# Performance work log

Measured on AMD Instinct MI355X. Metric: run time of the kernel, lower is better.

The kernel has to match this reference:

```python
import jax, jax.numpy as jnp
import numpy as np

N_ANGLES = 8


def setup_inputs() -> dict:
    key = jax.random.key(0)
    ks = jax.random.split(key, 6)
    N, in_size, out_size, K = 20000, 64, 64, 8
    M = N_ANGLES * N            # block-Laplacian dim = 160000
    E = M * 16                  # avg degree 16 -> 2.56M nnz
    x = jax.random.normal(ks[0], (N, in_size), dtype=jnp.float32)
    ls_vals = jax.random.normal(ks[1], (E,), dtype=jnp.float32) * 0.1
    ls_rows = jax.random.randint(ks[2], (E,), 0, M, dtype=jnp.int32)
    ls_cols = jax.random.randint(ks[3], (E,), 0, M, dtype=jnp.int32)
    weight = jax.random.normal(ks[4], (K, N_ANGLES * in_size, out_size), dtype=jnp.float32) * 0.05
    bias = jnp.zeros((out_size,), dtype=jnp.float32)
    return {"x": x, "ls_vals": ls_vals, "weight": weight, "bias": bias,
            "ls_rows": ls_rows, "ls_cols": ls_cols}


def reference(x, ls_vals, weight, bias, ls_rows, ls_cols):
    N, in_size = x.shape
    K = weight.shape[0]
    M = N_ANGLES * N

    def spmm(T):
        # sparse [M,M] @ dense [M,in] via gather + segment_sum
        return jax.ops.segment_sum(ls_vals[:, None] * T[ls_cols], ls_rows,
                                   num_segments=M)

    def feat(T):
        # [n_angles*N, in] -> [N, n_angles*in] (angle-major per node)
        return T.reshape(N_ANGLES, N, in_size).transpose(1, 0, 2).reshape(N, -1)

    Tx0 = jnp.tile(x, (N_ANGLES, 1))                  # [M, in]
    out = feat(Tx0) @ weight[0]                       # [N, out]
    Tx1 = spmm(Tx0)
    out = out + feat(Tx1) @ weight[1]
    for k in range(2, K):
        Tx2 = 2.0 * spmm(Tx1) - Tx0
        out = out + feat(Tx2) @ weight[k]
        Tx0, Tx1 = Tx1, Tx2
    return out + bias
```

## Files before the change

kernel.cpp:

```cpp
#include <hip/hip_runtime.h>
#include <hip/hip_bf16.h>

#define N_NODES 20000
#define NANG 8
#define CH 64
#define M_ROWS (NANG * N_NODES)
#define E_EDGES (M_ROWS * 16)
#define K_CHEB 8
#define WK_STRIDE (NANG * CH * CH)
#define BROWS 256
#define NB (M_ROWS / BROWS)
#define NCHUNK 512
#define CHUNK (E_EDGES / NCHUNK)
#define SCAN_K (NCHUNK / 256)
#define SC_RE 20
#define RPW 4
#define SPMM_BLOCKS (M_ROWS / (4 * RPW))
#define KCAT 3648
#define SK_TOTAL 114
#define BCAP 5120
#define GROWS 32
#define GEMM_BLOCKS (N_NODES / GROWS)

typedef short short8 __attribute__((ext_vector_type(8)));
typedef float f32x4 __attribute__((ext_vector_type(4)));

__device__ __forceinline__ float bf2f(ushort u) {
    return __uint_as_float((unsigned int)u << 16);
}


__global__ __launch_bounds__(256) void count_kernel(const int* __restrict__ rows,
                                                    int* __restrict__ chunk_cnt) {
    __shared__ int h[NB];
    int c = blockIdx.x, tid = threadIdx.x;
    for (int i = tid; i < NB; i += 256) h[i] = 0;
    __syncthreads();
    int base = c * CHUNK;
    for (int i = tid; i < CHUNK; i += 256) atomicAdd(&h[rows[base + i] >> 8], 1);
    __syncthreads();
    for (int i = tid; i < NB; i += 256) chunk_cnt[(size_t)c * NB + i] = h[i];
}

__global__ __launch_bounds__(256) void bscan2_kernel(int* __restrict__ chunk_cnt,
                                                     int* __restrict__ btotal) {
    __shared__ int s[256];
    int b = blockIdx.x, t = threadIdx.x;
    int loc[SCAN_K];
    int sum = 0;
#pragma unroll
    for (int k = 0; k < SCAN_K; ++k) {
        loc[k] = chunk_cnt[(size_t)(t * SCAN_K + k) * NB + b];
        sum += loc[k];
    }
    s[t] = sum;
    __syncthreads();
#pragma unroll
    for (int off = 1; off < 256; off <<= 1) {
        int u = (t >= off) ? s[t - off] : 0;
        __syncthreads();
        s[t] += u;
        __syncthreads();
    }
    int run = s[t] - sum;
#pragma unroll
    for (int k = 0; k < SCAN_K; ++k) {
        chunk_cnt[(size_t)(t * SCAN_K + k) * NB + b] = run;
        run += loc[k];
    }
    if (t == 255) btotal[b] = s[255];
}

__global__ void bscan_kernel(const int* __restrict__ btotal, int* __restrict__ bstart) {
    __shared__ int s[1024];
    int t = threadIdx.x;
    int v = (t < NB) ? btotal[t] : 0;
    s[t] = v;
    __syncthreads();
    for (int off = 1; off < 1024; off <<= 1) {
        int u = (t >= off) ? s[t - off] : 0;
        __syncthreads();
        s[t] += u;
        __syncthreads();
    }
    if (t < NB) bstart[t] = s[t] - v;
    if (t == 1023) bstart[NB] = s[1023];
}


__global__ __launch_bounds__(256) void scatter_kernel(
        const int* __restrict__ rows, const int* __restrict__ cols,
        const float* __restrict__ vals, const int* __restrict__ chunk_cnt,
        const int* __restrict__ bstart, int2* __restrict__ bedges) {
    __shared__ int2 stage[CHUNK];
    __shared__ ushort bkey[CHUNK];
    __shared__ int hist[NB];
    __shared__ int fill[NB];
    __shared__ int gaddr[NB];
    __shared__ int sc[256];
    int c = blockIdx.x, tid = threadIdx.x;
    for (int i = tid; i < NB; i += 256) hist[i] = 0;
    __syncthreads();

    int base = c * CHUNK;
    int2 eds[SC_RE];
    int keys[SC_RE];
#pragma unroll
    for (int k = 0; k < SC_RE; ++k) {
        int i = tid + k * 256;
        if (i < CHUNK) {
            int e = base + i;
            int r = rows[e];
            eds[k] = make_int2(cols[e] | ((r & 255) << 18), __float_as_int(vals[e]));
            keys[k] = r >> 8;
            atomicAdd(&hist[keys[k]], 1);
        } else keys[k] = -1;
    }
    __syncthreads();

    int loc[3];
    int sum = 0;
    int b0 = tid * 3;
#pragma unroll
    for (int k = 0; k < 3; ++k) {
        int b = b0 + k;
        loc[k] = (b < NB) ? hist[b] : 0;
        sum += loc[k];
    }
    sc[tid] = sum;
    __syncthreads();
#pragma unroll
    for (int off = 1; off < 256; off <<= 1) {
        int u = (tid >= off) ? sc[tid - off] : 0;
        __syncthreads();
        sc[tid] += u;
        __syncthreads();
    }
    int run = sc[tid] - sum;
#pragma unroll
    for (int k = 0; k < 3; ++k) {
        int b = b0 + k;
        if (b < NB) {
            fill[b] = run;
            gaddr[b] = bstart[b] + chunk_cnt[(size_t)c * NB + b] - run;
        }
        run += loc[k];
    }
    __syncthreads();

#pragma unroll
    for (int k = 0; k < SC_RE; ++k) {
        if (keys[k] >= 0) {
            int p = atomicAdd(&fill[keys[k]], 1);
            stage[p] = eds[k];
            bkey[p] = (ushort)keys[k];
        }
    }
    __syncthreads();

    for (int i = tid; i < CHUNK; i += 256) {
        int b = bkey[i];
        bedges[gaddr[b] + i] = stage[i];
    }
}

__global__ __launch_bounds__(256) void bucket_group_kernel(
        const int* __restrict__ bstart, const int2* __restrict__ bin,
        int2* __restrict__ bout, int* __restrict__ row_start) {
    __shared__ int cnt[BROWS];
    __shared__ int pref[BROWS];
    __shared__ int fill[BROWS];
    __shared__ int2 ob[BCAP];
    int b = blockIdx.x, tid = threadIdx.x;
    int s = bstart[b], e = bstart[b + 1];
    int n = e - s;
    cnt[tid] = 0;
    __syncthreads();
    int2 eds[20];
    int ni = 0;
    for (int i = tid; i < n; i += 256, ++ni) {
        int2 ed = bin[s + i];
        if (ni < 20) eds[ni] = ed;
        atomicAdd(&cnt[(ed.x >> 18) & 255], 1);
    }
    __syncthreads();
    int v = cnt[tid];
    pref[tid] = v;
    __syncthreads();
#pragma unroll
    for (int off = 1; off < 256; off <<= 1) {
        int u = (tid >= off) ? pref[tid - off] : 0;
        __syncthreads();
        pref[tid] += u;
        __syncthreads();
    }
    int my_excl = pref[tid] - v;
    __syncthreads();
    pref[tid] = my_excl;
    fill[tid] = my_excl;
    __syncthreads();

    if (n <= BCAP) {
        ni = 0;
        for (int i = tid; i < n; i += 256, ++ni) {
            int2 ed = (ni < 20) ? eds[ni] : bin[s + i];
            int p = atomicAdd(&fill[(ed.x >> 18) & 255], 1);
            ob[p] = make_int2(ed.x & 0x3ffff, ed.y);
        }
        __syncthreads();
        for (int i = tid; i < n; i += 256)
            bout[s + i] = ob[i];
    } else {
        ni = 0;
        for (int i = tid; i < n; i += 256, ++ni) {
            int2 ed = (ni < 20) ? eds[ni] : bin[s + i];
            int p = atomicAdd(&fill[(ed.x >> 18) & 255], 1);
            bout[s + p] = make_int2(ed.x & 0x3ffff, ed.y);
        }
    }
    row_start[b * BROWS + tid] = s + pref[tid];
    if (b == NB - 1 && tid == 0) row_start[M_ROWS] = e;
}


__global__ void xconv_kernel(const float* __restrict__ x, ushort* __restrict__ xb) {
    int i = blockIdx.x * 256 + threadIdx.x;
    __hip_bfloat16 v = __float2bfloat16(x[i]);
    xb[i] = *(ushort*)&v;
}

__global__ void wcat_kernel(const float* __restrict__ W, ushort* __restrict__ Wcat) {
    int idx = blockIdx.x * 256 + threadIdx.x;
    int n   = idx / KCAT;
    int kkc = idx - n * KCAT;
    float v;
    if (kkc < 64) {
        v = 0.f;
#pragma unroll
        for (int a = 0; a < NANG; ++a) v += W[(a * 64 + kkc) * 64 + n];
    } else {
        int k  = ((kkc - 64) >> 9) + 1;
        int kk = (kkc - 64) & 511;
        v = W[(size_t)k * WK_STRIDE + kk * 64 + n];
    }
    __hip_bfloat16 b = __float2bfloat16(v);
    Wcat[idx] = *(ushort*)&b;
}


template <int TIN_TILED, int TSUB_MODE>
__global__ __launch_bounds__(256) void spmm_kernel(
        const int* __restrict__ row_start, const int2* __restrict__ edges,
        const ushort* __restrict__ Tin, const ushort* __restrict__ Tsub,
        ushort* __restrict__ Tout, float alpha, float beta) {
    int wid = (blockIdx.x * 256 + threadIdx.x) >> 6;
    int lane = threadIdx.x & 63;
    int r0 = wid * RPW;
    int l16 = lane & 15;

    int sb[RPW + 1];
#pragma unroll
    for (int j = 0; j <= RPW; ++j)
        sb[j] = __builtin_amdgcn_readfirstlane(row_start[r0 + j]);

    int2 ed[RPW];
#pragma unroll
    for (int j = 0; j < RPW; ++j) {
        int idx = min(sb[j] + l16, sb[j + 1] - 1);
        idx = max(idx, 0);
        ed[j] = edges[idx];
    }

#pragma unroll
    for (int j = 0; j < RPW; ++j) {
        int s = sb[j], e = sb[j + 1];
        float acc0 = 0.f, acc1 = 0.f;
        int2 cur = ed[j];
        for (int base = s; base < e; base += 16) {
            int2 nxt = cur;
            if (base + 16 < e) {
                int idx = min(base + 16 + l16, e - 1);
                nxt = edges[idx];
            }
            ushort raw[16];
#pragma unroll
            for (int i = 0; i < 16; ++i) {
                unsigned c = (unsigned)__builtin_amdgcn_readlane(cur.x, i);
                if (TIN_TILED) c %= N_NODES;
                raw[i] = Tin[(size_t)c * CH + lane];
            }
#pragma unroll
            for (int i = 0; i < 16; ++i) {
                int wbits = __builtin_amdgcn_readlane(cur.y, i);
                if (base + i >= e) wbits = 0;
                float t = bf2f(raw[i]);
                if (i & 1) acc1 = fmaf(__int_as_float(wbits), t, acc1);
                else       acc0 = fmaf(__int_as_float(wbits), t, acc0);
            }
            cur = nxt;
        }
        int r = r0 + j;
        float v = alpha * (acc0 + acc1);
        size_t oi = (size_t)r * CH + lane;
        if (TSUB_MODE == 1) v += beta * bf2f(Tsub[oi]);
        if (TSUB_MODE == 2) v += beta * bf2f(Tsub[(size_t)((unsigned)r % N_NODES) * CH + lane]);
        __hip_bfloat16 o = __float2bfloat16(v);
        Tout[oi] = *(ushort*)&o;
    }
}


__global__ __launch_bounds__(256) void gemm_cat_kernel(
        const ushort* __restrict__ xb,
        const ushort* __restrict__ Tall,
        const ushort* __restrict__ Wcat,
        const float* __restrict__ bias,
        float* __restrict__ out) {
    __shared__ float red[4][16][64];
    int m0 = blockIdx.x * GROWS;
    int w = threadIdx.x >> 6;
    int l = threadIdx.x & 63;
    int lm = l & 15;
    int lq = l >> 4;
    const short* Xp = (const short*)xb;
    const short* Tp = (const short*)Tall;
    const short* Wp = (const short*)Wcat;

    f32x4 acc[2][4];
#pragma unroll
    for (int rg = 0; rg < 2; ++rg)
#pragma unroll
        for (int t = 0; t < 4; ++t) acc[rg][t] = (f32x4){0.f, 0.f, 0.f, 0.f};

    auto LDA = [&](int sk, int rg) -> short8 {
        int u = sk - 2;
        return *(const short8*)(Tp
            + ((size_t)(u >> 4) * M_ROWS + (size_t)((u & 15) >> 1) * N_NODES
               + (m0 + rg * 16 + lm)) * CH
            + (u & 1) * 32 + lq * 8);
    };
    auto LDB = [&](int sk, int t) -> short8 {
        return *(const short8*)(Wp + (size_t)(t * 16 + lm) * KCAT + sk * 32 + lq * 8);
    };

    if (w == 0) {
#pragma unroll
        for (int sk = 0; sk < 2; ++sk) {
            short8 a0 = *(const short8*)(Xp + (size_t)(m0 + lm) * CH + sk * 32 + lq * 8);
            short8 a1 = *(const short8*)(Xp + (size_t)(m0 + 16 + lm) * CH + sk * 32 + lq * 8);
#pragma unroll
            for (int t = 0; t < 4; ++t) {
                short8 bf = LDB(sk, t);
                acc[0][t] = __builtin_amdgcn_mfma_f32_16x16x32_bf16(a0, bf, acc[0][t], 0, 0, 0);
                acc[1][t] = __builtin_amdgcn_mfma_f32_16x16x32_bf16(a1, bf, acc[1][t], 0, 0, 0);
            }
        }
    }

    int tb = 2 + w * 28;
#pragma unroll 2
    for (int i = 0; i < 28; ++i) {
        int sk = tb + i;
        short8 a0 = LDA(sk, 0);
        short8 a1 = LDA(sk, 1);
#pragma unroll
        for (int t = 0; t < 4; ++t) {
            short8 bf = LDB(sk, t);
            acc[0][t] = __builtin_amdgcn_mfma_f32_16x16x32_bf16(a0, bf, acc[0][t], 0, 0, 0);
            acc[1][t] = __builtin_amdgcn_mfma_f32_16x16x32_bf16(a1, bf, acc[1][t], 0, 0, 0);
        }
    }

#pragma unroll
    for (int rg = 0; rg < 2; ++rg) {
        if (rg) __syncthreads();
#pragma unroll
        for (int t = 0; t < 4; ++t)
#pragma unroll
            for (int rI = 0; rI < 4; ++rI) red[w][t * 4 + rI][l] = acc[rg][t][rI];
        __syncthreads();
        int col = w * 16 + lm;
        float b = bias[col];
#pragma unroll
        for (int rI = 0; rI < 4; ++rI) {
            int i2 = w * 4 + rI;
            float sum = red[0][i2][l] + red[1][i2][l] + red[2][i2][l] + red[3][i2][l];
            out[(size_t)(m0 + rg * 16 + lq * 4 + rI) * CH + col] = sum + b;
        }
    }
}


extern "C" void kernel_launch(void* const* d_in, const int* in_sizes, int n_in,
                              void* d_out, int out_size, void* d_ws, size_t ws_size,
                              hipStream_t stream) {
    (void)in_sizes; (void)n_in; (void)out_size; (void)ws_size;
    const float* x       = (const float*)d_in[0];
    const float* ls_vals = (const float*)d_in[1];
    const float* weight  = (const float*)d_in[2];
    const float* bias    = (const float*)d_in[3];
    const int*   ls_rows = (const int*)d_in[4];
    const int*   ls_cols = (const int*)d_in[5];
    float* out = (float*)d_out;

    char* ws = (char*)d_ws;
    size_t off = 0;
    auto alloc = [&](size_t bytes) -> void* {
        void* p = ws + off;
        off += (bytes + 255) & ~(size_t)255;
        return p;
    };
    int*  chunk_cnt = (int*)alloc((size_t)NCHUNK * NB * sizeof(int));
    int*  btotal    = (int*)alloc(NB * sizeof(int));
    int*  bstart    = (int*)alloc((NB + 1) * sizeof(int));
    int*  row_start = (int*)alloc((M_ROWS + 1) * sizeof(int));
    int2* bedges2   = (int2*)alloc((size_t)E_EDGES * sizeof(int2));
    ushort* Wcat = (ushort*)alloc((size_t)64 * KCAT * sizeof(ushort));
    ushort* xb   = (ushort*)alloc((size_t)N_NODES * CH * sizeof(ushort));
    ushort* Tall = (ushort*)alloc((size_t)7 * M_ROWS * CH * sizeof(ushort));
    int2* bedges = (int2*)Tall;

    count_kernel<<<NCHUNK, 256, 0, stream>>>(ls_rows, chunk_cnt);
    bscan2_kernel<<<NB, 256, 0, stream>>>(chunk_cnt, btotal);
    bscan_kernel<<<1, 1024, 0, stream>>>(btotal, bstart);
    scatter_kernel<<<NCHUNK, 256, 0, stream>>>(ls_rows, ls_cols, ls_vals, chunk_cnt,
                                               bstart, bedges);
    bucket_group_kernel<<<NB, 256, 0, stream>>>(bstart, bedges, bedges2, row_start);

    xconv_kernel<<<(N_NODES * CH) / 256, 256, 0, stream>>>(x, xb);
    wcat_kernel<<<(64 * KCAT) / 256, 256, 0, stream>>>(weight, Wcat);

    ushort* T[8];
    for (int k = 1; k < K_CHEB; ++k) T[k] = Tall + (size_t)(k - 1) * M_ROWS * CH;

    spmm_kernel<1, 0><<<SPMM_BLOCKS, 256, 0, stream>>>(
        row_start, bedges2, xb, xb, T[1], 1.f, 0.f);
    spmm_kernel<0, 2><<<SPMM_BLOCKS, 256, 0, stream>>>(
        row_start, bedges2, T[1], xb, T[2], 2.f, -1.f);
    for (int k = 3; k < K_CHEB; ++k) {
        spmm_kernel<0, 1><<<SPMM_BLOCKS, 256, 0, stream>>>(
            row_start, bedges2, T[k - 1], T[k - 2], T[k], 2.f, -1.f);
    }

    gemm_cat_kernel<<<GEMM_BLOCKS, 256, 0, stream>>>(xb, Tall, Wcat, bias, out);
}
```

Before: 572.6 us.

## Split final GEMM into per-order segment GEMMs interleaved with SpMM launches

Replaces the single large concatenated GEMM at the end with a templated segment GEMM launched after each Chebyshev SpMM step, accumulating into the output. The intent is to consume each T_k while it is still hot in cache (MI355X has a large last-level cache) instead of rereading all seven T buffers from HBM at the end. In exchange it adds seven extra kernel launches and read-modify-write traffic on the fp32 output, and each small GEMM may underfill the GPU.

Result: slower. 602.2 us (+5.2%).

```diff
diff --git a/kernel.cpp b/kernel.cpp
--- a/kernel.cpp
+++ b/kernel.cpp
@@ -310,20 +310,20 @@
 }
 
 
-__global__ __launch_bounds__(256) void gemm_cat_kernel(
-        const ushort* __restrict__ xb,
-        const ushort* __restrict__ Tall,
+template <int NSK, int INIT>
+__global__ __launch_bounds__(256) void gemm_seg_kernel(
+        const ushort* __restrict__ Aseg,
         const ushort* __restrict__ Wcat,
         const float* __restrict__ bias,
-        float* __restrict__ out) {
+        float* __restrict__ out,
+        int skbase) {
     __shared__ float red[4][16][64];
     int m0 = blockIdx.x * GROWS;
     int w = threadIdx.x >> 6;
     int l = threadIdx.x & 63;
     int lm = l & 15;
     int lq = l >> 4;
-    const short* Xp = (const short*)xb;
-    const short* Tp = (const short*)Tall;
+    const short* Ap = (const short*)Aseg;
     const short* Wp = (const short*)Wcat;
 
     f32x4 acc[2][4];
@@ -332,40 +332,25 @@
 #pragma unroll
         for (int t = 0; t < 4; ++t) acc[rg][t] = (f32x4){0.f, 0.f, 0.f, 0.f};
 
-    auto LDA = [&](int sk, int rg) -> short8 {
-        int u = sk - 2;
-        return *(const short8*)(Tp
-            + ((size_t)(u >> 4) * M_ROWS + (size_t)((u & 15) >> 1) * N_NODES
-               + (m0 + rg * 16 + lm)) * CH
-            + (u & 1) * 32 + lq * 8);
-    };
-    auto LDB = [&](int sk, int t) -> short8 {
-        return *(const short8*)(Wp + (size_t)(t * 16 + lm) * KCAT + sk * 32 + lq * 8);
-    };
-
-    if (w == 0) {
-#pragma unroll
-        for (int sk = 0; sk < 2; ++sk) {
-            short8 a0 = *(const short8*)(Xp + (size_t)(m0 + lm) * CH + sk * 32 + lq * 8);
-            short8 a1 = *(const short8*)(Xp + (size_t)(m0 + 16 + lm) * CH + sk * 32 + lq * 8);
-#pragma unroll
-            for (int t = 0; t < 4; ++t) {
-                short8 bf = LDB(sk, t);
-                acc[0][t] = __builtin_amdgcn_mfma_f32_16x16x32_bf16(a0, bf, acc[0][t], 0, 0, 0);
-                acc[1][t] = __builtin_amdgcn_mfma_f32_16x16x32_bf16(a1, bf, acc[1][t], 0, 0, 0);
-            }
-        }
-    }
-
-    int tb = 2 + w * 28;
+    constexpr int KPW = (NSK + 3) / 4;
+    int s0 = w * KPW;
+    int s1 = min(s0 + KPW, NSK);
 #pragma unroll 2
-    for (int i = 0; i < 28; ++i) {
-        int sk = tb + i;
-        short8 a0 = LDA(sk, 0);
-        short8 a1 = LDA(sk, 1);
+    for (int ks = s0; ks < s1; ++ks) {
+        int sk = skbase + ks;
+        short8 a0, a1;
+        if (INIT) {
+            a0 = *(const short8*)(Ap + (size_t)(m0 + lm) * CH + ks * 32 + lq * 8);
+            a1 = *(const short8*)(Ap + (size_t)(m0 + 16 + lm) * CH + ks * 32 + lq * 8);
+        } else {
+            const short* base = Ap + ((size_t)(ks >> 1) * N_NODES + m0 + lm) * CH
+                                + (ks & 1) * 32 + lq * 8;
+            a0 = *(const short8*)base;
+            a1 = *(const short8*)(base + (size_t)16 * CH);
+        }
 #pragma unroll
         for (int t = 0; t < 4; ++t) {
-            short8 bf = LDB(sk, t);
+            short8 bf = *(const short8*)(Wp + (size_t)(t * 16 + lm) * KCAT + sk * 32 + lq * 8);
             acc[0][t] = __builtin_amdgcn_mfma_f32_16x16x32_bf16(a0, bf, acc[0][t], 0, 0, 0);
             acc[1][t] = __builtin_amdgcn_mfma_f32_16x16x32_bf16(a1, bf, acc[1][t], 0, 0, 0);
         }
@@ -380,12 +365,13 @@
             for (int rI = 0; rI < 4; ++rI) red[w][t * 4 + rI][l] = acc[rg][t][rI];
         __syncthreads();
         int col = w * 16 + lm;
-        float b = bias[col];
 #pragma unroll
         for (int rI = 0; rI < 4; ++rI) {
             int i2 = w * 4 + rI;
             float sum = red[0][i2][l] + red[1][i2][l] + red[2][i2][l] + red[3][i2][l];
-            out[(size_t)(m0 + rg * 16 + lq * 4 + rI) * CH + col] = sum + b;
+            size_t idx = (size_t)(m0 + rg * 16 + lq * 4 + rI) * CH + col;
+            if (INIT) out[idx] = sum + bias[col];
+            else      out[idx] = out[idx] + sum;
         }
     }
 }
@@ -433,14 +419,20 @@
     ushort* T[8];
     for (int k = 1; k < K_CHEB; ++k) T[k] = Tall + (size_t)(k - 1) * M_ROWS * CH;
 
+    gemm_seg_kernel<2, 1><<<GEMM_BLOCKS, 256, 0, stream>>>(xb, Wcat, bias, out, 0);
+
     spmm_kernel<1, 0><<<SPMM_BLOCKS, 256, 0, stream>>>(
         row_start, bedges2, xb, xb, T[1], 1.f, 0.f);
+    gemm_seg_kernel<16, 0><<<GEMM_BLOCKS, 256, 0, stream>>>(T[1], Wcat, bias, out, 2);
+
     spmm_kernel<0, 2><<<SPMM_BLOCKS, 256, 0, stream>>>(
         row_start, bedges2, T[1], xb, T[2], 2.f, -1.f);
+    gemm_seg_kernel<16, 0><<<GEMM_BLOCKS, 256, 0, stream>>>(T[2], Wcat, bias, out, 18);
+
     for (int k = 3; k < K_CHEB; ++k) {
         spmm_kernel<0, 1><<<SPMM_BLOCKS, 256, 0, stream>>>(
             row_start, bedges2, T[k - 1], T[k - 2], T[k], 2.f, -1.f);
-    }
-
-    gemm_cat_kernel<<<GEMM_BLOCKS, 256, 0, stream>>>(xb, Tall, Wcat, bias, out);
-}
+        gemm_seg_kernel<16, 0><<<GEMM_BLOCKS, 256, 0, stream>>>(
+            T[k], Wcat, bias, out, 2 + 16 * (k - 1));
+    }
+}
```
